# Optimization experiments

Measured on AMD Instinct MI355X. Metric: run time of the kernel, lower is better.

Reference implementation:

```python
import jax, jax.numpy as jnp
import numpy as np

D_MODEL = 1024
NUM_HEADS = 16
D_FF = 4096
NEG_INF = -1e9


def _linear_params(key, d_in, d_out):
    kw, kb = jax.random.split(key)
    bound = 1.0 / np.sqrt(d_in)
    W = jax.random.uniform(kw, (d_in, d_out), jnp.float32, -bound, bound)
    b = jax.random.uniform(kb, (d_out,), jnp.float32, -bound, bound)
    return W, b


def setup_inputs() -> dict:
    key = jax.random.key(0)
    ks = jax.random.split(key, 8)
    B, S = 2, 2048
    x = jax.random.normal(ks[0], (B, S, D_MODEL), jnp.float32)
    # causal mask: 1 = attend, 0 = masked
    mask = jnp.tril(jnp.ones((S, S), jnp.bool_))[None, :, :]
    Wq, bq = _linear_params(ks[1], D_MODEL, D_MODEL)
    Wk, bk = _linear_params(ks[2], D_MODEL, D_MODEL)
    Wv, bv = _linear_params(ks[3], D_MODEL, D_MODEL)
    Wo, bo = _linear_params(ks[4], D_MODEL, D_MODEL)
    W1, b1 = _linear_params(ks[5], D_MODEL, D_FF)
    W2, b2 = _linear_params(ks[6], D_FF, D_MODEL)
    ln1_g = jnp.ones((D_MODEL,), jnp.float32)
    ln1_b = jnp.zeros((D_MODEL,), jnp.float32)
    ln2_g = jnp.ones((D_MODEL,), jnp.float32)
    ln2_b = jnp.zeros((D_MODEL,), jnp.float32)
    return {"x": x, "mask": mask,
            "Wq": Wq, "bq": bq, "Wk": Wk, "bk": bk, "Wv": Wv, "bv": bv,
            "Wo": Wo, "bo": bo, "W1": W1, "b1": b1, "W2": W2, "b2": b2,
            "ln1_g": ln1_g, "ln1_b": ln1_b, "ln2_g": ln2_g, "ln2_b": ln2_b}


def layer_norm(x, g, b, eps=1e-5):
    mu = jnp.mean(x, axis=-1, keepdims=True)
    var = jnp.mean(jnp.square(x - mu), axis=-1, keepdims=True)
    return (x - mu) * jax.lax.rsqrt(var + eps) * g + b


def attention(xn, mask, Wq, bq, Wk, bk, Wv, bv, Wo, bo):
    B, S, D = xn.shape
    H, dk = NUM_HEADS, D // NUM_HEADS
    q = (xn @ Wq + bq).reshape(B, S, H, dk).transpose(0, 2, 1, 3)  # [B,H,S,dk]
    k = (xn @ Wk + bk).reshape(B, S, H, dk).transpose(0, 2, 1, 3)
    v = (xn @ Wv + bv).reshape(B, S, H, dk).transpose(0, 2, 1, 3)
    scores = jnp.einsum("bhsd,bhtd->bhst", q, k) / jnp.sqrt(jnp.float32(dk))
    scores = jnp.where(mask[:, None, :, :], scores, NEG_INF)
    attn = jax.nn.softmax(scores, axis=-1)
    out = jnp.einsum("bhst,bhtd->bhsd", attn, v)  # [B,H,S,dk]
    out = out.transpose(0, 2, 1, 3).reshape(B, S, D)
    return out @ Wo + bo


def reference(x, mask, Wq, bq, Wk, bk, Wv, bv, Wo, bo, W1, b1, W2, b2,
              ln1_g, ln1_b, ln2_g, ln2_b):
    # pre-norm MHA + residual (dropout = identity at eval)
    h = x + attention(layer_norm(x, ln1_g, ln1_b), mask,
                      Wq, bq, Wk, bk, Wv, bv, Wo, bo)
    # pre-norm FFN + residual
    ff = jax.nn.relu(layer_norm(h, ln2_g, ln2_b) @ W1 + b1) @ W2 + b2
    return h + ff
```

## Files before the change

kernel.cpp:

```cpp
#include <hip/hip_runtime.h>

typedef unsigned short u16;
typedef __attribute__((ext_vector_type(8))) short    s16x8;
typedef __attribute__((ext_vector_type(8))) unsigned short u16x8;
typedef __attribute__((ext_vector_type(4))) float    f32x4;

typedef __attribute__((address_space(1))) const void gvoid_c;
typedef __attribute__((address_space(3))) void       lvoid;

__device__ __forceinline__ float b2f(u16 x) {
    return __builtin_bit_cast(float, (unsigned)x << 16);
}
__device__ __forceinline__ u16 f2bf(float f) {
    unsigned u = __builtin_bit_cast(unsigned, f);
    return (u16)((u + 0x7FFFu + ((u >> 16) & 1u)) >> 16);
}
__device__ __forceinline__ u16 f2bf_trunc(float f) {
    return (u16)(__builtin_bit_cast(unsigned, f) >> 16);
}
__device__ __forceinline__ void gld16(const void* g, void* l) {
    __builtin_amdgcn_global_load_lds((gvoid_c*)g, (lvoid*)l, 16, 0, 0);
}

__global__ __launch_bounds__(256) void transpose_all(
    const float* __restrict__ Wq, const float* __restrict__ Wk,
    const float* __restrict__ Wv, const float* __restrict__ Wo,
    const float* __restrict__ W1, const float* __restrict__ W2,
    const float* __restrict__ bq, const float* __restrict__ bk,
    const float* __restrict__ bv,
    u16* __restrict__ Wqkv_t, u16* __restrict__ Wo_t,
    u16* __restrict__ W1_t, u16* __restrict__ W2_t, float* __restrict__ bqkv)
{
    __shared__ u16 tile[32][33];
    int id = blockIdx.x;
    if (id >= 12288) {
        int i = (id - 12288) * 256 + threadIdx.x;
        bqkv[i] = (i < 1024) ? bq[i] : (i < 2048 ? bk[i - 1024] : bv[i - 2048]);
        return;
    }
    const float* src; u16* dst; int R, C, bx, by;
    if (id < 4096) {
        int m = id >> 10, r = id & 1023;
        bx = r & 31; by = r >> 5; R = 1024; C = 1024;
        src = (m == 0) ? Wq : (m == 1) ? Wk : (m == 2) ? Wv : Wo;
        dst = (m == 0) ? Wqkv_t : (m == 1) ? Wqkv_t + 1024 * 1024
            : (m == 2) ? Wqkv_t + 2048 * 1024 : Wo_t;
    } else if (id < 8192) {
        int r = id - 4096; bx = r & 127; by = r >> 7; R = 1024; C = 4096;
        src = W1; dst = W1_t;
    } else {
        int r = id - 8192; bx = r & 31; by = r >> 5; R = 4096; C = 1024;
        src = W2; dst = W2_t;
    }
    int tx = threadIdx.x & 31, ty = threadIdx.x >> 5;
    int c0 = bx * 32, r0 = by * 32;
#pragma unroll
    for (int i = 0; i < 32; i += 8)
        tile[ty + i][tx] = f2bf(src[(size_t)(r0 + ty + i) * C + c0 + tx]);
    __syncthreads();
#pragma unroll
    for (int i = 0; i < 32; i += 8)
        dst[(size_t)(c0 + ty + i) * R + r0 + tx] = tile[tx][ty + i];
}

__global__ __launch_bounds__(256) void ln_k(
    const float* __restrict__ in, const float* __restrict__ gg,
    const float* __restrict__ bb, u16* __restrict__ out)
{
    const int D = 1024;
    int row  = blockIdx.x * 4 + (threadIdx.x >> 6);
    int lane = threadIdx.x & 63;
    const float* ip = in + (size_t)row * D;
    float v[16];
#pragma unroll
    for (int cc = 0; cc < 4; cc++) {
        f32x4 t = *(const f32x4*)(ip + cc * 256 + lane * 4);
#pragma unroll
        for (int i = 0; i < 4; i++) v[cc * 4 + i] = t[i];
    }
    float s1 = 0.f, s2 = 0.f;
#pragma unroll
    for (int i = 0; i < 16; i++) { s1 += v[i]; s2 += v[i] * v[i]; }
#pragma unroll
    for (int m = 1; m < 64; m <<= 1) { s1 += __shfl_xor(s1, m); s2 += __shfl_xor(s2, m); }
    float mu   = s1 * (1.f / 1024.f);
    float var  = s2 * (1.f / 1024.f) - mu * mu;
    float rstd = rsqrtf(var + 1e-5f);
#pragma unroll
    for (int cc = 0; cc < 4; cc++) {
        int e = cc * 256 + lane * 4;
        f32x4 gv = *(const f32x4*)(gg + e);
        f32x4 bv = *(const f32x4*)(bb + e);
        u16 o[4];
#pragma unroll
        for (int i = 0; i < 4; i++)
            o[i] = f2bf((v[cc * 4 + i] - mu) * rstd * gv[i] + bv[i]);
        *(__attribute__((ext_vector_type(4))) unsigned short*)(out + (size_t)row * D + e) =
            (__attribute__((ext_vector_type(4))) unsigned short){o[0], o[1], o[2], o[3]};
    }
}

template <int BN, int RES, bool RELU, bool OUTF32>
__global__ __launch_bounds__(256) void gemm2(
    const u16* __restrict__ A, const u16* __restrict__ Bt,
    const float* __restrict__ bias, const float* __restrict__ res,
    void* __restrict__ out, int M, int N, int K)
{
    constexpr int NFR = BN / 32;
    __shared__ u16 As[2][4096];
    __shared__ u16 Bs[2][BN * 32];
    int tid = threadIdx.x, wave = tid >> 6, lane = tid & 63;
    int g = lane >> 4, c = lane & 15;
    int wm = wave >> 1, wn = wave & 1;

    int gx = gridDim.x, nwg = gx * gridDim.y;
    int id = blockIdx.y * gx + blockIdx.x;
    int swz = (id & 7) * (nwg >> 3) + (id >> 3);
    int m0 = (swz / gx) * 128, n0 = (swz % gx) * BN;

    f32x4 acc[4][NFR];
#pragma unroll
    for (int m = 0; m < 4; m++)
#pragma unroll
        for (int n = 0; n < NFR; n++) acc[m][n] = (f32x4){0, 0, 0, 0};

    int ch0 = wave * 128 + lane, ch1 = ch0 + 64;
    const u16* Ag0 = A + (size_t)(m0 + (ch0 >> 2)) * K + (ch0 & 3) * 8;
    const u16* Ag1 = A + (size_t)(m0 + (ch1 >> 2)) * K + (ch1 & 3) * 8;
    const u16* Bg0;
    const u16* Bg1 = nullptr;
    if constexpr (BN == 128) {
        Bg0 = Bt + (size_t)(n0 + (ch0 >> 2)) * K + (ch0 & 3) * 8;
        Bg1 = Bt + (size_t)(n0 + (ch1 >> 2)) * K + (ch1 & 3) * 8;
    } else {
        int chb = wave * 64 + lane;
        Bg0 = Bt + (size_t)(n0 + (chb >> 2)) * K + (chb & 3) * 8;
    }

    auto stage = [&](int buf, int kk) {
        gld16(Ag0 + kk, &As[buf][wave * 1024]);
        gld16(Ag1 + kk, &As[buf][wave * 1024 + 512]);
        if constexpr (BN == 128) {
            gld16(Bg0 + kk, &Bs[buf][wave * 1024]);
            gld16(Bg1 + kk, &Bs[buf][wave * 1024 + 512]);
        } else {
            gld16(Bg0 + kk, &Bs[buf][wave * 512]);
        }
    };

    int nt = K / 32;
    stage(0, 0);
    __syncthreads();
    int cur = 0;
    for (int t = 0; t < nt; t++) {
        if (t + 1 < nt) stage(cur ^ 1, (t + 1) * 32);
        s16x8 af[4], bfr[NFR];
#pragma unroll
        for (int m = 0; m < 4; m++)
            af[m] = *(const s16x8*)&As[cur][(wm * 64 + m * 16 + c) * 32 + g * 8];
#pragma unroll
        for (int n = 0; n < NFR; n++)
            bfr[n] = *(const s16x8*)&Bs[cur][(wn * (BN / 2) + n * 16 + c) * 32 + g * 8];
        __builtin_amdgcn_s_setprio(1);
#pragma unroll
        for (int m = 0; m < 4; m++)
#pragma unroll
            for (int n = 0; n < NFR; n++)
                acc[m][n] = __builtin_amdgcn_mfma_f32_16x16x32_bf16(af[m], bfr[n], acc[m][n], 0, 0, 0);
        __builtin_amdgcn_s_setprio(0);
        __syncthreads();
        cur ^= 1;
    }

#pragma unroll
    for (int n = 0; n < NFR; n++) {
        int col = n0 + wn * (BN / 2) + n * 16 + c;
        float bb = bias[col];
#pragma unroll
        for (int m = 0; m < 4; m++) {
#pragma unroll
            for (int j = 0; j < 4; j++) {
                int row = m0 + wm * 64 + m * 16 + g * 4 + j;
                float v = acc[m][n][j] + bb;
                if constexpr (RES == 2) v += res[(size_t)row * N + col];
                if constexpr (RELU) v = fmaxf(v, 0.f);
                if constexpr (OUTF32) ((float*)out)[(size_t)row * N + col] = v;
                else                  ((u16*)out)[(size_t)row * N + col] = f2bf(v);
            }
        }
    }
}

__global__ __launch_bounds__(256) void gemm_n64_k64(
    const u16* __restrict__ A, const u16* __restrict__ Bt,
    const float* __restrict__ bias, const float* __restrict__ res,
    float* __restrict__ out, int M, int N, int K)
{
    __shared__ u16 As[2][8192];
    __shared__ u16 Bs[2][4096];
    int tid = threadIdx.x, wave = tid >> 6, lane = tid & 63;
    int g = lane >> 4, c = lane & 15;
    int wm = wave >> 1, wn = wave & 1;

    int gx = gridDim.x, nwg = gx * gridDim.y;
    int id = blockIdx.y * gx + blockIdx.x;
    int swz = (id & 7) * (nwg >> 3) + (id >> 3);
    int m0 = (swz / gx) * 128, n0 = (swz % gx) * 64;

    f32x4 acc[4][2];
#pragma unroll
    for (int m = 0; m < 4; m++)
#pragma unroll
        for (int n = 0; n < 2; n++) acc[m][n] = (f32x4){0, 0, 0, 0};

    const u16* asrc[4];
#pragma unroll
    for (int k = 0; k < 4; k++) {
        int ch = k * 256 + tid, row = ch >> 3, c8 = ch & 7;
        asrc[k] = A + (size_t)(m0 + row) * K + ((c8 ^ (row & 7)) * 8);
    }
    const u16* bsrc[2];
#pragma unroll
    for (int k = 0; k < 2; k++) {
        int ch = k * 256 + tid, row = ch >> 3, c8 = ch & 7;
        bsrc[k] = Bt + (size_t)(n0 + row) * K + ((c8 ^ (row & 7)) * 8);
    }

    auto stage = [&](int buf, int k0) {
#pragma unroll
        for (int k = 0; k < 4; k++)
            gld16(asrc[k] + k0, &As[buf][(k * 256 + wave * 64) * 8]);
#pragma unroll
        for (int k = 0; k < 2; k++)
            gld16(bsrc[k] + k0, &Bs[buf][(k * 256 + wave * 64) * 8]);
    };

    int nt = K / 64;
    stage(0, 0);
    __syncthreads();
    int cur = 0;
    int x7 = c & 7;
    for (int t = 0; t < nt; t++) {
        if (t + 1 < nt) stage(cur ^ 1, (t + 1) * 64);
        s16x8 af[2][4], bfr[2][2];
#pragma unroll
        for (int kk = 0; kk < 2; kk++) {
#pragma unroll
            for (int m = 0; m < 4; m++)
                af[kk][m] = *(const s16x8*)&As[cur][(wm * 64 + m * 16 + c) * 64 + ((kk * 4 + g) ^ x7) * 8];
#pragma unroll
            for (int n = 0; n < 2; n++)
                bfr[kk][n] = *(const s16x8*)&Bs[cur][(wn * 32 + n * 16 + c) * 64 + ((kk * 4 + g) ^ x7) * 8];
        }
        __builtin_amdgcn_s_setprio(1);
#pragma unroll
        for (int kk = 0; kk < 2; kk++)
#pragma unroll
            for (int m = 0; m < 4; m++)
#pragma unroll
                for (int n = 0; n < 2; n++)
                    acc[m][n] = __builtin_amdgcn_mfma_f32_16x16x32_bf16(af[kk][m], bfr[kk][n], acc[m][n], 0, 0, 0);
        __builtin_amdgcn_s_setprio(0);
        __syncthreads();
        cur ^= 1;
    }

#pragma unroll
    for (int n = 0; n < 2; n++) {
        int col = n0 + wn * 32 + n * 16 + c;
        float bb = bias[col];
#pragma unroll
        for (int m = 0; m < 4; m++) {
#pragma unroll
            for (int j = 0; j < 4; j++) {
                int row = m0 + wm * 64 + m * 16 + g * 4 + j;
                out[(size_t)row * N + col] = acc[m][n][j] + bb + res[(size_t)row * N + col];
            }
        }
    }
}

__global__ __launch_bounds__(256) void v_transpose(
    const u16* __restrict__ qkv, u16* __restrict__ vt)
{
    const int S = 2048, NC = 3072;
    __shared__ u16 tile[64][72];
    int st = blockIdx.x, bh = blockIdx.y, b = bh >> 4, h = bh & 15;
    int tid = threadIdx.x;
    int i = tid >> 3, cb8 = (tid & 7) * 8;
    const u16* src = qkv + (size_t)(b * S + st * 64) * NC + 2048 + h * 64;
    u16x8 a0 = *(const u16x8*)(src + (size_t)i * NC + cb8);
    u16x8 a1 = *(const u16x8*)(src + (size_t)(i + 32) * NC + cb8);
    *(u16x8*)&tile[i][cb8]      = a0;
    *(u16x8*)&tile[i + 32][cb8] = a1;
    __syncthreads();
    int d = tid >> 3, e8 = (tid & 7) * 8;
    int m = (d & 7) * 8;
#pragma unroll
    for (int rr = 0; rr < 2; rr++) {
        int r = d + rr * 32;
        u16x8 o;
#pragma unroll
        for (int j = 0; j < 8; j++) o[j] = tile[(e8 ^ m) + j][r];
        *(u16x8*)(vt + ((size_t)bh * 64 + r) * 2048 + st * 64 + e8) = o;
    }
}

__global__ __launch_bounds__(256) void attn_fwd5(
    const u16* __restrict__ qkv, const u16* __restrict__ vt,
    u16* __restrict__ o)
{
    const int S = 2048, NC = 3072;
    __shared__ u16 Ks[2][4096];
    __shared__ u16 Vs[2][4096];
    __shared__ u16 Plds[4][16][64];
    int qt = 31 - blockIdx.x;
    int bh = blockIdx.y, b = bh >> 4, h = bh & 15;
    int tid = threadIdx.x, wave = tid >> 6, lane = tid & 63;
    int g = lane >> 4, c = lane & 15;
    int sr = tid >> 3, scb8 = (tid & 7) * 8;
    int mS = (sr & 7) * 8;
    int mR = (c & 7) * 8;
    int pW = ((g * 4) & 7) << 3;
    int pR = (c & 7) << 3;

    const u16* kbase = qkv + (size_t)b * S * NC + 1024 + h * 64;
    const u16* vbase = vt + (size_t)bh * 64 * 2048;

    auto stageKV = [&](int buf, int t0) {
        gld16(kbase + (size_t)(t0 + sr)      * NC + (scb8 ^ mS), &Ks[buf][wave * 512]);
        gld16(kbase + (size_t)(t0 + sr + 32) * NC + (scb8 ^ mS), &Ks[buf][2048 + wave * 512]);
        gld16(vbase + (size_t)sr        * 2048 + t0 + scb8, &Vs[buf][wave * 512]);
        gld16(vbase + (size_t)(sr + 32) * 2048 + t0 + scb8, &Vs[buf][2048 + wave * 512]);
    };

    int q0 = qt * 64 + wave * 16;
    const u16* qptr = qkv + (size_t)(b * S + q0 + c) * NC + h * 64;
    s16x8 qf0 = *(const s16x8*)(qptr + g * 8);
    s16x8 qf1 = *(const s16x8*)(qptr + 32 + g * 8);

    float mr[4], lr[4];
    f32x4 acc[4];
#pragma unroll
    for (int j = 0; j < 4; j++) { mr[j] = -1e30f; lr[j] = 0.f; }
#pragma unroll
    for (int n = 0; n < 4; n++) acc[n] = (f32x4){0, 0, 0, 0};

    auto do_tile = [&](int cur, int t0, bool masked) __attribute__((always_inline)) {
        f32x4 s[4];
        __builtin_amdgcn_s_setprio(1);
#pragma unroll
        for (int kt = 0; kt < 4; kt++) {
            int r = kt * 16 + c;
            s16x8 kf0 = *(const s16x8*)&Ks[cur][r * 64 + ((g * 8) ^ mR)];
            s16x8 kf1 = *(const s16x8*)&Ks[cur][r * 64 + ((32 + g * 8) ^ mR)];
            f32x4 sv = (f32x4){0, 0, 0, 0};
            sv = __builtin_amdgcn_mfma_f32_16x16x32_bf16(qf0, kf0, sv, 0, 0, 0);
            sv = __builtin_amdgcn_mfma_f32_16x16x32_bf16(qf1, kf1, sv, 0, 0, 0);
            s[kt] = sv;
        }
        __builtin_amdgcn_s_setprio(0);
#pragma unroll
        for (int kt = 0; kt < 4; kt++) {
#pragma unroll
            for (int j = 0; j < 4; j++) {
                if (masked) {
                    int kcol = t0 + kt * 16 + c;
                    int qrow = q0 + g * 4 + j;
                    s[kt][j] = (kcol <= qrow) ? s[kt][j] * 0.125f : -1e30f;
                } else {
                    s[kt][j] *= 0.125f;
                }
            }
        }
        float tm4[4];
#pragma unroll
        for (int j = 0; j < 4; j++) {
            float tm = fmaxf(fmaxf(s[0][j], s[1][j]), fmaxf(s[2][j], s[3][j]));
#pragma unroll
            for (int m = 1; m < 16; m <<= 1) tm = fmaxf(tm, __shfl_xor(tm, m));
            tm4[j] = tm;
        }
        bool grow = (tm4[0] > mr[0]) | (tm4[1] > mr[1]) | (tm4[2] > mr[2]) | (tm4[3] > mr[3]);
        if (__any(grow)) {
#pragma unroll
            for (int j = 0; j < 4; j++) {
                float mnew = fmaxf(mr[j], tm4[j]);
                float corr = __expf(mr[j] - mnew);
                mr[j] = mnew;
                lr[j] *= corr;
#pragma unroll
                for (int n = 0; n < 4; n++) acc[n][j] *= corr;
            }
        }
#pragma unroll
        for (int j = 0; j < 4; j++) {
            float rs = 0.f;
#pragma unroll
            for (int kt = 0; kt < 4; kt++) { float p = __expf(s[kt][j] - mr[j]); s[kt][j] = p; rs += p; }
#pragma unroll
            for (int m = 1; m < 16; m <<= 1) rs += __shfl_xor(rs, m);
            lr[j] += rs;
        }
#pragma unroll
        for (int kt = 0; kt < 4; kt++)
#pragma unroll
            for (int j = 0; j < 4; j++)
                Plds[wave][g * 4 + j][(kt * 16 + c) ^ (pW ^ ((j & 7) << 3) ? ((g * 4 + j) & 7) << 3 : ((g * 4 + j) & 7) << 3)] = f2bf_trunc(s[kt][j]);
        s16x8 pa0 = *(const s16x8*)&Plds[wave][c][(g * 8) ^ pR];
        s16x8 pa1 = *(const s16x8*)&Plds[wave][c][(32 + g * 8) ^ pR];
        __builtin_amdgcn_s_setprio(1);
#pragma unroll
        for (int n = 0; n < 4; n++) {
            int r = n * 16 + c;
            s16x8 vb0 = *(const s16x8*)&Vs[cur][r * 64 + ((g * 8) ^ mR)];
            s16x8 vb1 = *(const s16x8*)&Vs[cur][r * 64 + ((32 + g * 8) ^ mR)];
            acc[n] = __builtin_amdgcn_mfma_f32_16x16x32_bf16(pa0, vb0, acc[n], 0, 0, 0);
            acc[n] = __builtin_amdgcn_mfma_f32_16x16x32_bf16(pa1, vb1, acc[n], 0, 0, 0);
        }
        __builtin_amdgcn_s_setprio(0);
    };

    stageKV(0, 0);
    __syncthreads();
    int cur = 0;
    for (int t = 0; t < qt; t++) {
        stageKV(cur ^ 1, (t + 1) * 64);
        do_tile(cur, t * 64, false);
        __syncthreads();
        cur ^= 1;
    }
    do_tile(cur, qt * 64, true);

#pragma unroll
    for (int j = 0; j < 4; j++) {
        float inv = 1.f / lr[j];
        size_t rbase = (size_t)(b * S + q0 + g * 4 + j) * 1024 + h * 64;
#pragma unroll
        for (int n = 0; n < 4; n++)
            o[rbase + n * 16 + c] = f2bf(acc[n][j] * inv);
    }
}

extern "C" void kernel_launch(void* const* d_in, const int* in_sizes, int n_in,
                              void* d_out, int out_size, void* d_ws, size_t ws_size,
                              hipStream_t stream)
{
    const float* x    = (const float*)d_in[0];
    const float* Wq   = (const float*)d_in[2];  const float* bq = (const float*)d_in[3];
    const float* Wk   = (const float*)d_in[4];  const float* bk = (const float*)d_in[5];
    const float* Wv   = (const float*)d_in[6];  const float* bv = (const float*)d_in[7];
    const float* Wo   = (const float*)d_in[8];  const float* bo = (const float*)d_in[9];
    const float* W1   = (const float*)d_in[10]; const float* b1 = (const float*)d_in[11];
    const float* W2   = (const float*)d_in[12]; const float* b2 = (const float*)d_in[13];
    const float* ln1g = (const float*)d_in[14]; const float* ln1b = (const float*)d_in[15];
    const float* ln2g = (const float*)d_in[16]; const float* ln2b = (const float*)d_in[17];

    unsigned char* ws = (unsigned char*)d_ws;
    u16*   Wqkv_t = (u16*)(ws + 0);
    u16*   Wo_t   = (u16*)(ws + 6291456);
    u16*   W1_t   = (u16*)(ws + 8388608);
    u16*   W2_t   = (u16*)(ws + 16777216);
    float* bqkv   = (float*)(ws + 25165824);
    u16*   lnbuf  = (u16*)(ws + 25178112);
    u16*   qkvbuf = (u16*)(ws + 33566720);
    u16*   attnb  = (u16*)(ws + 58732544);
    u16*   f1buf  = (u16*)(ws + 33566720);
    float* hbuf   = (float*)(ws + 67121152);
    u16*   vtbuf  = (u16*)(ws + 67121152);

    transpose_all<<<12300, 256, 0, stream>>>(Wq, Wk, Wv, Wo, W1, W2, bq, bk, bv,
                                             Wqkv_t, Wo_t, W1_t, W2_t, bqkv);

    ln_k<<<1024, 256, 0, stream>>>(x, ln1g, ln1b, lnbuf);
    gemm2<128, 0, false, false><<<dim3(24, 32), 256, 0, stream>>>(
        lnbuf, Wqkv_t, bqkv, nullptr, qkvbuf, 4096, 3072, 1024);
    v_transpose<<<dim3(32, 32), 256, 0, stream>>>(qkvbuf, vtbuf);
    attn_fwd5<<<dim3(32, 32), 256, 0, stream>>>(qkvbuf, vtbuf, attnb);

    gemm_n64_k64<<<dim3(16, 32), 256, 0, stream>>>(
        attnb, Wo_t, bo, x, hbuf, 4096, 1024, 1024);

    ln_k<<<1024, 256, 0, stream>>>(hbuf, ln2g, ln2b, lnbuf);
    gemm2<128, 0, true, false><<<dim3(32, 32), 256, 0, stream>>>(
        lnbuf, W1_t, b1, nullptr, f1buf, 4096, 4096, 1024);
    gemm_n64_k64<<<dim3(16, 32), 256, 0, stream>>>(
        f1buf, W2_t, b2, hbuf, (float*)d_out, 4096, 1024, 4096);
}
```

Baseline: 435.8 us.

## Pair causal query tiles per block, prescale Q for exp2, use DPP reductions

The attention kernel now runs each block over a pair of query tiles (qp and 31-qp). Every block therefore does the same amount of causal work, and the grid is halved. The 1/sqrt(dk)·log2(e) scale is folded into the QKV GEMM epilogue for the Q columns, so the softmax can use raw v_exp_f32 (exp2) without a per-element multiply. Row max and row sum reductions move from shfl_xor to DPP row moves. The trade-off is fewer blocks (512) and therefore less occupancy slack, and Q is now stored pre-scaled in bf16, which adds rounding risk.

```diff
diff --git a/kernel.cpp b/kernel.cpp
--- a/kernel.cpp
+++ b/kernel.cpp
@@ -20,6 +20,31 @@
 }
 __device__ __forceinline__ void gld16(const void* g, void* l) {
     __builtin_amdgcn_global_load_lds((gvoid_c*)g, (lvoid*)l, 16, 0, 0);
+}
+__device__ __forceinline__ float fexp2(float x) {
+    float r; asm("v_exp_f32 %0, %1" : "=v"(r) : "v"(x)); return r;
+}
+__device__ __forceinline__ float dpp_max16(float x) {
+    int v = __builtin_bit_cast(int, x);
+    x = fmaxf(x, __builtin_bit_cast(float, __builtin_amdgcn_mov_dpp(v, 0xB1, 0xF, 0xF, true)));
+    v = __builtin_bit_cast(int, x);
+    x = fmaxf(x, __builtin_bit_cast(float, __builtin_amdgcn_mov_dpp(v, 0x4E, 0xF, 0xF, true)));
+    v = __builtin_bit_cast(int, x);
+    x = fmaxf(x, __builtin_bit_cast(float, __builtin_amdgcn_mov_dpp(v, 0x124, 0xF, 0xF, true)));
+    v = __builtin_bit_cast(int, x);
+    x = fmaxf(x, __builtin_bit_cast(float, __builtin_amdgcn_mov_dpp(v, 0x128, 0xF, 0xF, true)));
+    return x;
+}
+__device__ __forceinline__ float dpp_sum16(float x) {
+    int v = __builtin_bit_cast(int, x);
+    x = x + __builtin_bit_cast(float, __builtin_amdgcn_mov_dpp(v, 0xB1, 0xF, 0xF, true));
+    v = __builtin_bit_cast(int, x);
+    x = x + __builtin_bit_cast(float, __builtin_amdgcn_mov_dpp(v, 0x4E, 0xF, 0xF, true));
+    v = __builtin_bit_cast(int, x);
+    x = x + __builtin_bit_cast(float, __builtin_amdgcn_mov_dpp(v, 0x124, 0xF, 0xF, true));
+    v = __builtin_bit_cast(int, x);
+    x = x + __builtin_bit_cast(float, __builtin_amdgcn_mov_dpp(v, 0x128, 0xF, 0xF, true));
+    return x;
 }
 
 __global__ __launch_bounds__(256) void transpose_all(
@@ -100,7 +125,7 @@
     }
 }
 
-template <int BN, int RES, bool RELU, bool OUTF32>
+template <int BN, int RES, bool RELU, bool OUTF32, int QSC = 0>
 __global__ __launch_bounds__(256) void gemm2(
     const u16* __restrict__ A, const u16* __restrict__ Bt,
     const float* __restrict__ bias, const float* __restrict__ res,
@@ -182,6 +207,7 @@
             for (int j = 0; j < 4; j++) {
                 int row = m0 + wm * 64 + m * 16 + g * 4 + j;
                 float v = acc[m][n][j] + bb;
+                if constexpr (QSC) { if (col < 1024) v *= 0.18033688f; }
                 if constexpr (RES == 2) v += res[(size_t)row * N + col];
                 if constexpr (RELU) v = fmaxf(v, 0.f);
                 if constexpr (OUTF32) ((float*)out)[(size_t)row * N + col] = v;
@@ -306,7 +332,7 @@
     }
 }
 
-__global__ __launch_bounds__(256) void attn_fwd5(
+__global__ __launch_bounds__(256) void attn_fwd6(
     const u16* __restrict__ qkv, const u16* __restrict__ vt,
     u16* __restrict__ o)
 {
@@ -314,14 +340,12 @@
     __shared__ u16 Ks[2][4096];
     __shared__ u16 Vs[2][4096];
     __shared__ u16 Plds[4][16][64];
-    int qt = 31 - blockIdx.x;
-    int bh = blockIdx.y, b = bh >> 4, h = bh & 15;
+    int qp = blockIdx.x, bh = blockIdx.y, b = bh >> 4, h = bh & 15;
     int tid = threadIdx.x, wave = tid >> 6, lane = tid & 63;
     int g = lane >> 4, c = lane & 15;
     int sr = tid >> 3, scb8 = (tid & 7) * 8;
     int mS = (sr & 7) * 8;
     int mR = (c & 7) * 8;
-    int pW = ((g * 4) & 7) << 3;
     int pR = (c & 7) << 3;
 
     const u16* kbase = qkv + (size_t)b * S * NC + 1024 + h * 64;
@@ -334,111 +358,112 @@
         gld16(vbase + (size_t)(sr + 32) * 2048 + t0 + scb8, &Vs[buf][2048 + wave * 512]);
     };
 
-    int q0 = qt * 64 + wave * 16;
-    const u16* qptr = qkv + (size_t)(b * S + q0 + c) * NC + h * 64;
-    s16x8 qf0 = *(const s16x8*)(qptr + g * 8);
-    s16x8 qf1 = *(const s16x8*)(qptr + 32 + g * 8);
-
-    float mr[4], lr[4];
-    f32x4 acc[4];
-#pragma unroll
-    for (int j = 0; j < 4; j++) { mr[j] = -1e30f; lr[j] = 0.f; }
-#pragma unroll
-    for (int n = 0; n < 4; n++) acc[n] = (f32x4){0, 0, 0, 0};
-
-    auto do_tile = [&](int cur, int t0, bool masked) __attribute__((always_inline)) {
-        f32x4 s[4];
-        __builtin_amdgcn_s_setprio(1);
-#pragma unroll
-        for (int kt = 0; kt < 4; kt++) {
-            int r = kt * 16 + c;
-            s16x8 kf0 = *(const s16x8*)&Ks[cur][r * 64 + ((g * 8) ^ mR)];
-            s16x8 kf1 = *(const s16x8*)&Ks[cur][r * 64 + ((32 + g * 8) ^ mR)];
-            f32x4 sv = (f32x4){0, 0, 0, 0};
-            sv = __builtin_amdgcn_mfma_f32_16x16x32_bf16(qf0, kf0, sv, 0, 0, 0);
-            sv = __builtin_amdgcn_mfma_f32_16x16x32_bf16(qf1, kf1, sv, 0, 0, 0);
-            s[kt] = sv;
+#pragma unroll 1
+    for (int ph = 0; ph < 2; ph++) {
+        int qt = ph ? qp : 31 - qp;
+        int q0 = qt * 64 + wave * 16;
+        const u16* qptr = qkv + (size_t)(b * S + q0 + c) * NC + h * 64;
+        s16x8 qf0 = *(const s16x8*)(qptr + g * 8);
+        s16x8 qf1 = *(const s16x8*)(qptr + 32 + g * 8);
+
+        float mr[4], lr[4];
+        f32x4 acc[4];
+#pragma unroll
+        for (int j = 0; j < 4; j++) { mr[j] = -1e30f; lr[j] = 0.f; }
+#pragma unroll
+        for (int n = 0; n < 4; n++) acc[n] = (f32x4){0, 0, 0, 0};
+
+        auto do_tile = [&](int cur, int t0, bool masked) __attribute__((always_inline)) {
+            f32x4 s[4];
+            __builtin_amdgcn_s_setprio(1);
+#pragma unroll
+            for (int kt = 0; kt < 4; kt++) {
+                int r = kt * 16 + c;
+                s16x8 kf0 = *(const s16x8*)&Ks[cur][r * 64 + ((g * 8) ^ mR)];
+                s16x8 kf1 = *(const s16x8*)&Ks[cur][r * 64 + ((32 + g * 8) ^ mR)];
+                f32x4 sv = (f32x4){0, 0, 0, 0};
+                sv = __builtin_amdgcn_mfma_f32_16x16x32_bf16(qf0, kf0, sv, 0, 0, 0);
+                sv = __builtin_amdgcn_mfma_f32_16x16x32_bf16(qf1, kf1, sv, 0, 0, 0);
+                s[kt] = sv;
+            }
+            __builtin_amdgcn_s_setprio(0);
+            if (masked) {
+#pragma unroll
+                for (int kt = 0; kt < 4; kt++) {
+                    int kcol = t0 + kt * 16 + c;
+#pragma unroll
+                    for (int j = 0; j < 4; j++) {
+                        int qrow = q0 + g * 4 + j;
+                        if (kcol > qrow) s[kt][j] = -1e30f;
+                    }
+                }
+            }
+            float tm4[4];
+#pragma unroll
+            for (int j = 0; j < 4; j++)
+                tm4[j] = dpp_max16(fmaxf(fmaxf(s[0][j], s[1][j]), fmaxf(s[2][j], s[3][j])));
+            bool grow = (tm4[0] > mr[0]) | (tm4[1] > mr[1]) | (tm4[2] > mr[2]) | (tm4[3] > mr[3]);
+            if (__any(grow)) {
+#pragma unroll
+                for (int j = 0; j < 4; j++) {
+                    float mnew = fmaxf(mr[j], tm4[j]);
+                    float corr = fexp2(mr[j] - mnew);
+                    mr[j] = mnew;
+                    lr[j] *= corr;
+#pragma unroll
+                    for (int n = 0; n < 4; n++) acc[n][j] *= corr;
+                }
+            }
+#pragma unroll
+            for (int j = 0; j < 4; j++) {
+                float p0 = fexp2(s[0][j] - mr[j]);
+                float p1 = fexp2(s[1][j] - mr[j]);
+                float p2 = fexp2(s[2][j] - mr[j]);
+                float p3 = fexp2(s[3][j] - mr[j]);
+                s[0][j] = p0; s[1][j] = p1; s[2][j] = p2; s[3][j] = p3;
+                lr[j] += dpp_sum16(((p0 + p1) + (p2 + p3)));
+            }
+#pragma unroll
+            for (int kt = 0; kt < 4; kt++)
+#pragma unroll
+                for (int j = 0; j < 4; j++) {
+                    int row = g * 4 + j;
+                    Plds[wave][row][(kt * 16 + c) ^ ((row & 7) << 3)] = f2bf_trunc(s[kt][j]);
+                }
+            s16x8 pa0 = *(const s16x8*)&Plds[wave][c][(g * 8) ^ pR];
+            s16x8 pa1 = *(const s16x8*)&Plds[wave][c][(32 + g * 8) ^ pR];
+            __builtin_amdgcn_s_setprio(1);
+#pragma unroll
+            for (int n = 0; n < 4; n++) {
+                int r = n * 16 + c;
+                s16x8 vb0 = *(const s16x8*)&Vs[cur][r * 64 + ((g * 8) ^ mR)];
+                s16x8 vb1 = *(const s16x8*)&Vs[cur][r * 64 + ((32 + g * 8) ^ mR)];
+                acc[n] = __builtin_amdgcn_mfma_f32_16x16x32_bf16(pa0, vb0, acc[n], 0, 0, 0);
+                acc[n] = __builtin_amdgcn_mfma_f32_16x16x32_bf16(pa1, vb1, acc[n], 0, 0, 0);
+            }
+            __builtin_amdgcn_s_setprio(0);
+        };
+
+        __syncthreads();
+        stageKV(0, 0);
+        __syncthreads();
+        int cur = 0;
+        for (int t = 0; t < qt; t++) {
+            stageKV(cur ^ 1, (t + 1) * 64);
+            do_tile(cur, t * 64, false);
+            __syncthreads();
+            cur ^= 1;
         }
-        __builtin_amdgcn_s_setprio(0);
-#pragma unroll
-        for (int kt = 0; kt < 4; kt++) {
-#pragma unroll
-            for (int j = 0; j < 4; j++) {
-                if (masked) {
-                    int kcol = t0 + kt * 16 + c;
-                    int qrow = q0 + g * 4 + j;
-                    s[kt][j] = (kcol <= qrow) ? s[kt][j] * 0.125f : -1e30f;
-                } else {
-                    s[kt][j] *= 0.125f;
-                }
-            }
+        do_tile(cur, qt * 64, true);
+
+#pragma unroll
+        for (int j = 0; j < 4; j++) {
+            float inv = 1.f / lr[j];
+            size_t rbase = (size_t)(b * S + q0 + g * 4 + j) * 1024 + h * 64;
+#pragma unroll
+            for (int n = 0; n < 4; n++)
+                o[rbase + n * 16 + c] = f2bf(acc[n][j] * inv);
         }
-        float tm4[4];
-#pragma unroll
-        for (int j = 0; j < 4; j++) {
-            float tm = fmaxf(fmaxf(s[0][j], s[1][j]), fmaxf(s[2][j], s[3][j]));
-#pragma unroll
-            for (int m = 1; m < 16; m <<= 1) tm = fmaxf(tm, __shfl_xor(tm, m));
-            tm4[j] = tm;
-        }
-        bool grow = (tm4[0] > mr[0]) | (tm4[1] > mr[1]) | (tm4[2] > mr[2]) | (tm4[3] > mr[3]);
-        if (__any(grow)) {
-#pragma unroll
-            for (int j = 0; j < 4; j++) {
-                float mnew = fmaxf(mr[j], tm4[j]);
-                float corr = __expf(mr[j] - mnew);
-                mr[j] = mnew;
-                lr[j] *= corr;
-#pragma unroll
-                for (int n = 0; n < 4; n++) acc[n][j] *= corr;
-            }
-        }
-#pragma unroll
-        for (int j = 0; j < 4; j++) {
-            float rs = 0.f;
-#pragma unroll
-            for (int kt = 0; kt < 4; kt++) { float p = __expf(s[kt][j] - mr[j]); s[kt][j] = p; rs += p; }
-#pragma unroll
-            for (int m = 1; m < 16; m <<= 1) rs += __shfl_xor(rs, m);
-            lr[j] += rs;
-        }
-#pragma unroll
-        for (int kt = 0; kt < 4; kt++)
-#pragma unroll
-            for (int j = 0; j < 4; j++)
-                Plds[wave][g * 4 + j][(kt * 16 + c) ^ (pW ^ ((j & 7) << 3) ? ((g * 4 + j) & 7) << 3 : ((g * 4 + j) & 7) << 3)] = f2bf_trunc(s[kt][j]);
-        s16x8 pa0 = *(const s16x8*)&Plds[wave][c][(g * 8) ^ pR];
-        s16x8 pa1 = *(const s16x8*)&Plds[wave][c][(32 + g * 8) ^ pR];
-        __builtin_amdgcn_s_setprio(1);
-#pragma unroll
-        for (int n = 0; n < 4; n++) {
-            int r = n * 16 + c;
-            s16x8 vb0 = *(const s16x8*)&Vs[cur][r * 64 + ((g * 8) ^ mR)];
-            s16x8 vb1 = *(const s16x8*)&Vs[cur][r * 64 + ((32 + g * 8) ^ mR)];
-            acc[n] = __builtin_amdgcn_mfma_f32_16x16x32_bf16(pa0, vb0, acc[n], 0, 0, 0);
-            acc[n] = __builtin_amdgcn_mfma_f32_16x16x32_bf16(pa1, vb1, acc[n], 0, 0, 0);
-        }
-        __builtin_amdgcn_s_setprio(0);
-    };
-
-    stageKV(0, 0);
-    __syncthreads();
-    int cur = 0;
-    for (int t = 0; t < qt; t++) {
-        stageKV(cur ^ 1, (t + 1) * 64);
-        do_tile(cur, t * 64, false);
-        __syncthreads();
-        cur ^= 1;
-    }
-    do_tile(cur, qt * 64, true);
-
-#pragma unroll
-    for (int j = 0; j < 4; j++) {
-        float inv = 1.f / lr[j];
-        size_t rbase = (size_t)(b * S + q0 + g * 4 + j) * 1024 + h * 64;
-#pragma unroll
-        for (int n = 0; n < 4; n++)
-            o[rbase + n * 16 + c] = f2bf(acc[n][j] * inv);
     }
 }
 
@@ -473,10 +498,10 @@
                                              Wqkv_t, Wo_t, W1_t, W2_t, bqkv);
 
     ln_k<<<1024, 256, 0, stream>>>(x, ln1g, ln1b, lnbuf);
-    gemm2<128, 0, false, false><<<dim3(24, 32), 256, 0, stream>>>(
+    gemm2<128, 0, false, false, 1><<<dim3(24, 32), 256, 0, stream>>>(
         lnbuf, Wqkv_t, bqkv, nullptr, qkvbuf, 4096, 3072, 1024);
     v_transpose<<<dim3(32, 32), 256, 0, stream>>>(qkvbuf, vtbuf);
-    attn_fwd5<<<dim3(32, 32), 256, 0, stream>>>(qkvbuf, vtbuf, attnb);
+    attn_fwd6<<<dim3(16, 32), 256, 0, stream>>>(qkvbuf, vtbuf, attnb);
 
     gemm_n64_k64<<<dim3(16, 32), 256, 0, stream>>>(
         attnb, Wo_t, bo, x, hbuf, 4096, 1024, 1024);
```

New measurement: 374.1 us. 14.2% less time.
